# Kernel tuning notes

Hardware: AMD Instinct MI355X
Metric: run time of the kernel (lower is better)

## Reference

```python
import jax, jax.numpy as jnp
import numpy as np

B, N, M, K = 4, 8192, 2048, 8
F1, F2 = 256, 256


def _knn_idx(p1t, p2t, k):
    # p1t [B,N,3], p2t [B,M,3] -> idx [B,N,k] of k nearest points in p2t for each p1t point
    d = (jnp.sum(p1t ** 2, -1)[:, :, None]
         + jnp.sum(p2t ** 2, -1)[:, None, :]
         - 2.0 * jnp.einsum('bnc,bmc->bnm', p1t, p2t))
    _, idx = jax.lax.top_k(-d, k)
    return idx


def _gather(feat, idx):
    # feat [B,C,M], idx [B,N,K] -> [B,C,N,K]  (grouping_operation)
    return jax.vmap(lambda f, i: f[:, i])(feat, idx)


def setup_inputs() -> dict:
    key = jax.random.key(0)
    ks = jax.random.split(key, 16)
    rn = lambda k, s: jax.random.normal(k, s, dtype=jnp.float32)
    ru = lambda k, s: jax.random.uniform(k, s, dtype=jnp.float32)
    return {
        'pos1': rn(ks[0], (B, 3, N)),
        'pos2': rn(ks[1], (B, 3, M)),
        'feature1': rn(ks[2], (B, F1, N)),
        'feature2': rn(ks[3], (B, F2, M)),
        'w1_0': rn(ks[4], (128, F2 + 3)) * 0.05, 's1_0': ru(ks[5], (128,)), 'b1_0': rn(ks[6], (128,)) * 0.05,
        'w1_1': rn(ks[7], (128, 128)) * 0.05, 's1_1': ru(ks[8], (128,)), 'b1_1': rn(ks[9], (128,)) * 0.05,
        'w1_2': rn(ks[10], (256, 128)) * 0.05, 's1_2': ru(ks[11], (256,)), 'b1_2': rn(ks[12], (256,)) * 0.05,
        'w2_0': rn(ks[13], (256, 256 + F1)) * 0.05, 's2_0': ru(ks[14], (256,)), 'b2_0': rn(ks[15], (256,)) * 0.05,
    }


def reference(pos1, pos2, feature1, feature2,
              w1_0, s1_0, b1_0, w1_1, s1_1, b1_1, w1_2, s1_2, b1_2,
              w2_0, s2_0, b2_0):
    # KNN grouping (knn=True branch): neighbors of each pos1 point among pos2 points
    idx = _knn_idx(pos1.transpose(0, 2, 1), pos2.transpose(0, 2, 1), K)  # [B,N,K]
    pos2_grouped = _gather(pos2, idx)                 # [B,3,N,K]
    pos_diff = pos2_grouped - pos1[:, :, :, None]     # [B,3,N,K]
    feat2_grouped = _gather(feature2, idx)            # [B,F2,N,K]
    feat = jnp.concatenate([feat2_grouped, pos_diff], axis=1)  # [B,F2+3,N,K]
    # mlp1: 1x1 Conv2d (no bias) + BN(eval, folded scale/bias) + ReLU
    for w, s, b in ((w1_0, s1_0, b1_0), (w1_1, s1_1, b1_1), (w1_2, s1_2, b1_2)):
        feat = jax.nn.relu(jnp.einsum('oc,bcnk->bonk', w, feat)
                           * s[None, :, None, None] + b[None, :, None, None])
    feat = jnp.max(feat, axis=-1)                     # [B,256,N]
    feat = jnp.concatenate([feat, feature1], axis=1)  # [B,256+F1,N]
    # mlp2: 1x1 Conv1d (no bias) + BN + ReLU
    for w, s, b in ((w2_0, s2_0, b2_0),):
        feat = jax.nn.relu(jnp.einsum('oc,bcn->bon', w, feat)
                           * s[None, :, None] + b[None, :, None])
    return feat
```

## Files before the change

### kernel.cpp

```cpp
#include <hip/hip_runtime.h>
#include <hip/hip_bf16.h>

#define B_ 4
#define N_ 8192
#define M_ 2048
#define K_ 8

typedef __bf16 bf16x8 __attribute__((ext_vector_type(8)));
typedef __bf16 bf16x4 __attribute__((ext_vector_type(4)));
typedef float  floatx4 __attribute__((ext_vector_type(4)));
typedef unsigned long long u64k;

__global__ __launch_bounds__(256) void prep_weights(
    const float* __restrict__ w10, const float* __restrict__ w11,
    const float* __restrict__ w12, const float* __restrict__ w20,
    __bf16* __restrict__ w0p, __bf16* __restrict__ w11b,
    __bf16* __restrict__ w12b, __bf16* __restrict__ w20b)
{
  int t = blockIdx.x * 256 + threadIdx.x;
  if (t < 36864) {
    int o = t / 288, c = t - o * 288;
    w0p[t] = (c < 259) ? (__bf16)w10[o * 259 + c] : (__bf16)0.0f;
  } else if (t < 53248) {
    int i = t - 36864; w11b[i] = (__bf16)w11[i];
  } else if (t < 86016) {
    int i = t - 53248; w12b[i] = (__bf16)w12[i];
  } else if (t < 217088) {
    int i = t - 86016; w20b[i] = (__bf16)w20[i];
  }
}

__global__ __launch_bounds__(256) void transpose_cast(
    const float* __restrict__ in, __bf16* __restrict__ out, int C, int L)
{
  __shared__ float tile[32][33];
  const int b = blockIdx.z;
  const int c0 = blockIdx.y * 32, l0 = blockIdx.x * 32;
  const int tx = threadIdx.x & 31, ty = threadIdx.x >> 5;
  const float* src = in + (size_t)b * C * L;
  #pragma unroll
  for (int i = 0; i < 4; i++)
    tile[ty + 8 * i][tx] = src[(size_t)(c0 + ty + 8 * i) * L + l0 + tx];
  __syncthreads();
  __bf16* dst = out + (size_t)b * L * C;
  #pragma unroll
  for (int i = 0; i < 4; i++)
    dst[(size_t)(l0 + ty + 8 * i) * C + c0 + tx] = (__bf16)tile[tx][ty + 8 * i];
}

__device__ __forceinline__ void ce(u64k& a, u64k& b) {
  u64k lo = a < b ? a : b;
  u64k hi = a < b ? b : a;
  a = lo; b = hi;
}

__global__ __launch_bounds__(256, 4) void knn_kernel(
    const float* __restrict__ pos1, const float* __restrict__ pos2,
    u64k* __restrict__ part)
{
  __shared__ floatx4 P[1024];
  __shared__ u64k md[64][33];
  const int b = blockIdx.y;
  const int half = blockIdx.z;
  const int n0 = blockIdx.x * 64;
  const int tid = threadIdx.x;
  const int cbase = half * 1024;

  const float* p2 = pos2 + b * 3 * M_;
  for (int i = tid; i < 1024; i += 256) {
    const int c = cbase + i;
    float x = p2[c], y = p2[M_ + c], z = p2[2 * M_ + c];
    floatx4 q;
    q[0] = x; q[1] = y; q[2] = z;
    q[3] = __fadd_rn(__fadd_rn(__fmul_rn(x, x), __fmul_rn(y, y)), __fmul_rn(z, z));
    P[i] = q;
  }
  __syncthreads();

  const int p = tid >> 2, t = tid & 3;
  const int n = n0 + p;
  const float* p1 = pos1 + b * 3 * N_;
  const float x1 = p1[n], y1 = p1[N_ + n], z1 = p1[2 * N_ + n];
  const float r1 = __fadd_rn(__fadd_rn(__fmul_rn(x1, x1), __fmul_rn(y1, y1)),
                             __fmul_rn(z1, z1));

  u64k bd[8];
  #pragma unroll
  for (int r = 0; r < 8; r++) bd[r] = ~0ULL;

  for (int bb = 0; bb < 32; ++bb) {
    floatx4 q[8];
    #pragma unroll
    for (int i = 0; i < 8; i++) q[i] = P[4 * (8 * bb + i) + t];

    u64k s[8];
    #pragma unroll
    for (int i = 0; i < 8; i++) {
      float dot = __fadd_rn(__fadd_rn(__fmul_rn(x1, q[i][0]), __fmul_rn(y1, q[i][1])),
                            __fmul_rn(z1, q[i][2]));
      float d = __fsub_rn(__fadd_rn(r1, q[i][3]), __fmul_rn(2.0f, dot));
      unsigned du = __float_as_uint(d);
      unsigned k32 = du ^ ((unsigned)((int)du >> 31) | 0x80000000u);
      s[i] = ((u64k)k32 << 11) | (unsigned)(cbase + 4 * (8 * bb + i) + t);
    }

    ce(s[0], s[1]); ce(s[2], s[3]); ce(s[4], s[5]); ce(s[6], s[7]);
    ce(s[0], s[2]); ce(s[1], s[3]); ce(s[4], s[6]); ce(s[5], s[7]);
    ce(s[1], s[2]); ce(s[5], s[6]);
    ce(s[0], s[4]); ce(s[1], s[5]); ce(s[2], s[6]); ce(s[3], s[7]);
    ce(s[2], s[4]); ce(s[3], s[5]);
    ce(s[1], s[2]); ce(s[3], s[4]); ce(s[5], s[6]);

    if (s[0] < bd[7]) {
      #pragma unroll
      for (int k = 0; k < 8; k++) { u64k x = s[7 - k]; bd[k] = bd[k] < x ? bd[k] : x; }
      ce(bd[0], bd[4]); ce(bd[1], bd[5]); ce(bd[2], bd[6]); ce(bd[3], bd[7]);
      ce(bd[0], bd[2]); ce(bd[1], bd[3]); ce(bd[4], bd[6]); ce(bd[5], bd[7]);
      ce(bd[0], bd[1]); ce(bd[2], bd[3]); ce(bd[4], bd[5]); ce(bd[6], bd[7]);
    }
  }

  #pragma unroll
  for (int r = 0; r < 8; r++) md[p][t * 8 + r] = bd[r];
  __syncthreads();

  if (tid < 64) {
    int h0 = 0, h1 = 0, h2 = 0, h3 = 0;
    u64k* o = part + ((size_t)((b * 2 + half) * N_ + n0 + tid)) * 8;
    #pragma unroll
    for (int r = 0; r < 8; r++) {
      u64k k0 = md[tid][h0], k1 = md[tid][8 + h1];
      u64k k2 = md[tid][16 + h2], k3 = md[tid][24 + h3];
      u64k m01 = k0 < k1 ? k0 : k1;
      u64k m23 = k2 < k3 ? k2 : k3;
      u64k m = m01 < m23 ? m01 : m23;
      h0 += (k0 == m); h1 += (k1 == m); h2 += (k2 == m); h3 += (k3 == m);
      o[r] = m;
    }
  }
}

__global__ __launch_bounds__(256) void knn_merge(
    const u64k* __restrict__ part, int* __restrict__ idx_out)
{
  const int pt = blockIdx.x * 256 + threadIdx.x;
  const int b = pt >> 13, n = pt & (N_ - 1);
  const u64k* a0 = part + ((size_t)((b * 2 + 0) * N_ + n)) * 8;
  const u64k* a1 = part + ((size_t)((b * 2 + 1) * N_ + n)) * 8;
  u64k av[8], cv[8];
  #pragma unroll
  for (int r = 0; r < 8; r++) { av[r] = a0[r]; cv[r] = a1[r]; }
  #pragma unroll
  for (int k = 0; k < 8; k++) { u64k x = cv[7 - k]; av[k] = av[k] < x ? av[k] : x; }
  ce(av[0], av[4]); ce(av[1], av[5]); ce(av[2], av[6]); ce(av[3], av[7]);
  ce(av[0], av[2]); ce(av[1], av[3]); ce(av[4], av[6]); ce(av[5], av[7]);
  ce(av[0], av[1]); ce(av[2], av[3]); ce(av[4], av[5]); ce(av[6], av[7]);
  int* o = idx_out + (size_t)pt * 8;
  #pragma unroll
  for (int r = 0; r < 8; r++) o[r] = (int)(av[r] & 2047u);
}

template <int KSTEPS>
__device__ __forceinline__ void mfma_layer_lds(
    const __bf16* X, const __bf16* W, int wstride,
    const float* sv, const float* bv,
    __bf16* Y, int ycolbase, int c0, int lane)
{
  const int lrow = lane & 15, quad = lane >> 4;
  floatx4 acc[4][2];
  const floatx4 fz = {0.f, 0.f, 0.f, 0.f};
  #pragma unroll
  for (int pt = 0; pt < 4; pt++) { acc[pt][0] = fz; acc[pt][1] = fz; }

  bf16x8 wf0 = *(const bf16x8*)(W + (size_t)(c0 + lrow) * wstride + quad * 8);
  bf16x8 wf1 = *(const bf16x8*)(W + (size_t)(c0 + 16 + lrow) * wstride + quad * 8);
  bf16x8 xf[4];
  #pragma unroll
  for (int pt = 0; pt < 4; pt++)
    xf[pt] = *(const bf16x8*)(X + (pt * 16 + lrow) * 136 + quad * 8);

  #pragma unroll
  for (int ks = 0; ks < KSTEPS; ks++) {
    bf16x8 wn0, wn1, xn[4];
    if (ks + 1 < KSTEPS) {
      const int kn = (ks + 1) * 32 + quad * 8;
      wn0 = *(const bf16x8*)(W + (size_t)(c0 + lrow) * wstride + kn);
      wn1 = *(const bf16x8*)(W + (size_t)(c0 + 16 + lrow) * wstride + kn);
      #pragma unroll
      for (int pt = 0; pt < 4; pt++)
        xn[pt] = *(const bf16x8*)(X + (pt * 16 + lrow) * 136 + kn);
    }
    #pragma unroll
    for (int pt = 0; pt < 4; pt++) {
      acc[pt][0] = __builtin_amdgcn_mfma_f32_16x16x32_bf16(wf0, xf[pt], acc[pt][0], 0, 0, 0);
      acc[pt][1] = __builtin_amdgcn_mfma_f32_16x16x32_bf16(wf1, xf[pt], acc[pt][1], 0, 0, 0);
    }
    if (ks + 1 < KSTEPS) {
      wf0 = wn0; wf1 = wn1;
      #pragma unroll
      for (int pt = 0; pt < 4; pt++) xf[pt] = xn[pt];
    }
  }

  #pragma unroll
  for (int pt = 0; pt < 4; pt++) {
    #pragma unroll
    for (int wt = 0; wt < 2; wt++) {
      const int colg = c0 + wt * 16 + quad * 4;
      floatx4 s4 = *(const floatx4*)(sv + colg);
      floatx4 b4 = *(const floatx4*)(bv + colg);
      bf16x4 pk;
      #pragma unroll
      for (int r = 0; r < 4; r++) {
        float v = acc[pt][wt][r] * s4[r] + b4[r];
        pk[r] = (__bf16)(v > 0.f ? v : 0.f);
      }
      *(bf16x4*)(Y + (pt * 16 + lrow) * 136 + (colg - ycolbase)) = pk;
    }
  }
}

__global__ __launch_bounds__(256, 3) void mlp1_kernel(
    const float* __restrict__ pos1, const float* __restrict__ pos2,
    const int* __restrict__ idx, const __bf16* __restrict__ f2t,
    const __bf16* __restrict__ w0p, const float* __restrict__ s10, const float* __restrict__ b10,
    const __bf16* __restrict__ w11b, const float* __restrict__ s11, const float* __restrict__ b11,
    const __bf16* __restrict__ w12b, const float* __restrict__ s12, const float* __restrict__ b12,
    __bf16* __restrict__ maxed)
{
  __shared__ __align__(16) __bf16 Xs[64 * 256];
  __shared__ __align__(16) __bf16 Y0[64 * 136];
  __shared__ int mrow[64];
  __shared__ __align__(16) float dp[64][4];
  __bf16* const Y1 = Xs;

  const int b = blockIdx.y;
  const int n0 = blockIdx.x * 8;
  const int tid = threadIdx.x;
  const int wave = tid >> 6, lane = tid & 63;
  const int lrow = lane & 15, quad = lane >> 4;
  const int c0 = 32 * wave;

  if (tid < 64) {
    const int r = tid, g = r >> 3;
    const int m = idx[(b * N_ + n0) * K_ + r];
    mrow[r] = m;
    const int n = n0 + g;
    dp[r][0] = pos2[b * 3 * M_ + m]          - pos1[b * 3 * N_ + n];
    dp[r][1] = pos2[b * 3 * M_ + M_ + m]     - pos1[b * 3 * N_ + N_ + n];
    dp[r][2] = pos2[b * 3 * M_ + 2 * M_ + m] - pos1[b * 3 * N_ + 2 * N_ + n];
    dp[r][3] = 0.f;
  }
  __syncthreads();

  {
    const int r0 = wave * 16;
    const int half = lane >> 5;
    const int ch = lane & 31;
    #pragma unroll
    for (int i = 0; i < 8; i++) {
      const int r = r0 + 2 * i + half;
      const int m = mrow[r];
      const char* src = (const char*)f2t
          + (((size_t)(b * M_ + m)) << 9)
          + ((ch << 4) ^ ((r & 7) << 4));
      __builtin_amdgcn_global_load_lds(
          (const __attribute__((address_space(1))) unsigned int*)src,
          (__attribute__((address_space(3))) unsigned int*)(Xs + (r0 + 2 * i) * 256),
          16, 0, 0);
    }
  }

  bf16x8 xlast[4];
  #pragma unroll
  for (int pt = 0; pt < 4; pt++) {
    bf16x8 v = {};
    if (quad == 0) {
      floatx4 d = *(const floatx4*)(&dp[pt * 16 + lrow][0]);
      v[0] = (__bf16)d[0]; v[1] = (__bf16)d[1]; v[2] = (__bf16)d[2];
    }
    xlast[pt] = v;
  }

  bf16x8 wf0 = *(const bf16x8*)(w0p + (size_t)(c0 + lrow) * 288 + quad * 8);
  bf16x8 wf1 = *(const bf16x8*)(w0p + (size_t)(c0 + 16 + lrow) * 288 + quad * 8);

  __syncthreads();

  {
    floatx4 acc[4][2];
    const floatx4 fz = {0.f, 0.f, 0.f, 0.f};
    #pragma unroll
    for (int pt = 0; pt < 4; pt++) { acc[pt][0] = fz; acc[pt][1] = fz; }

    const int swz = (lrow & 7) << 4;
    bf16x8 xf[4];
    #pragma unroll
    for (int pt = 0; pt < 4; pt++)
      xf[pt] = *(const bf16x8*)((const char*)Xs + (pt * 16 + lrow) * 512
                                + ((quad * 16) ^ swz));

    #pragma unroll
    for (int ks = 0; ks < 9; ks++) {
      bf16x8 wn0, wn1, xn[4];
      if (ks < 8) {
        const int kn = (ks + 1) * 32 + quad * 8;
        wn0 = *(const bf16x8*)(w0p + (size_t)(c0 + lrow) * 288 + kn);
        wn1 = *(const bf16x8*)(w0p + (size_t)(c0 + 16 + lrow) * 288 + kn);
        if (ks < 7) {
          const int kb = ((ks + 1) * 64 + quad * 16) ^ swz;
          #pragma unroll
          for (int pt = 0; pt < 4; pt++)
            xn[pt] = *(const bf16x8*)((const char*)Xs + (pt * 16 + lrow) * 512 + kb);
        } else {
          #pragma unroll
          for (int pt = 0; pt < 4; pt++) xn[pt] = xlast[pt];
        }
      }
      #pragma unroll
      for (int pt = 0; pt < 4; pt++) {
        acc[pt][0] = __builtin_amdgcn_mfma_f32_16x16x32_bf16(wf0, xf[pt], acc[pt][0], 0, 0, 0);
        acc[pt][1] = __builtin_amdgcn_mfma_f32_16x16x32_bf16(wf1, xf[pt], acc[pt][1], 0, 0, 0);
      }
      if (ks < 8) {
        wf0 = wn0; wf1 = wn1;
        #pragma unroll
        for (int pt = 0; pt < 4; pt++) xf[pt] = xn[pt];
      }
    }
    #pragma unroll
    for (int pt = 0; pt < 4; pt++) {
      #pragma unroll
      for (int wt = 0; wt < 2; wt++) {
        const int colg = c0 + wt * 16 + quad * 4;
        floatx4 s4 = *(const floatx4*)(s10 + colg);
        floatx4 b4 = *(const floatx4*)(b10 + colg);
        bf16x4 pk;
        #pragma unroll
        for (int r = 0; r < 4; r++) {
          float v = acc[pt][wt][r] * s4[r] + b4[r];
          pk[r] = (__bf16)(v > 0.f ? v : 0.f);
        }
        *(bf16x4*)(Y0 + (pt * 16 + lrow) * 136 + colg) = pk;
      }
    }
  }
  __syncthreads();

  mfma_layer_lds<4>(Y0, w11b, 128, s11, b11, Y1, 0, c0, lane);
  __syncthreads();

  #pragma unroll
  for (int p = 0; p < 2; p++) {
    mfma_layer_lds<4>(Y1, w12b, 128, s12, b12, Y0, 128 * p, 128 * p + c0, lane);
    __syncthreads();
    if (tid < 128) {
      const int g = tid >> 4, cb = (tid & 15) * 8;
      bf16x8 v0 = *(const bf16x8*)(Y0 + (g * 8) * 136 + cb);
      float fmx[8];
      #pragma unroll
      for (int j = 0; j < 8; j++) fmx[j] = (float)v0[j];
      #pragma unroll
      for (int k = 1; k < 8; k++) {
        bf16x8 v = *(const bf16x8*)(Y0 + (g * 8 + k) * 136 + cb);
        #pragma unroll
        for (int j = 0; j < 8; j++) {
          float f = (float)v[j];
          fmx[j] = f > fmx[j] ? f : fmx[j];
        }
      }
      bf16x8 o;
      #pragma unroll
      for (int j = 0; j < 8; j++) o[j] = (__bf16)fmx[j];
      *(bf16x8*)(maxed + ((size_t)(b * N_ + n0 + g)) * 256 + 128 * p + cb) = o;
    }
    __syncthreads();
  }
}

__global__ __launch_bounds__(256, 6) void mlp2_kernel(
    const __bf16* __restrict__ maxed, const __bf16* __restrict__ f1t,
    const __bf16* __restrict__ w20b, const float* __restrict__ s20,
    const float* __restrict__ b20, float* __restrict__ out)
{
  const int rows0 = blockIdx.x * 32;
  const int b = rows0 >> 13;
  const int nbase = rows0 & (N_ - 1);
  const int tid = threadIdx.x;
  const int wave = tid >> 6, lane = tid & 63;
  const int lrow = lane & 15, quad = lane >> 4;
  const int c0 = 128 * blockIdx.y + 32 * wave;
  const floatx4 fz = {0.f, 0.f, 0.f, 0.f};

  floatx4 acc[2][2];
  acc[0][0] = fz; acc[0][1] = fz; acc[1][0] = fz; acc[1][1] = fz;

  auto aptr = [&](int ks, int mt) -> const __bf16* {
    const int k = ks * 32 + quad * 8;
    return (ks < 8) ? (maxed + (size_t)(rows0 + mt * 16 + lrow) * 256 + k)
                    : (f1t + (size_t)(rows0 + mt * 16 + lrow) * 256 + (k - 256));
  };

  bf16x8 w0 = *(const bf16x8*)(w20b + (size_t)(c0 + lrow) * 512 + quad * 8);
  bf16x8 w1 = *(const bf16x8*)(w20b + (size_t)(c0 + 16 + lrow) * 512 + quad * 8);
  bf16x8 a0 = *(const bf16x8*)aptr(0, 0);
  bf16x8 a1 = *(const bf16x8*)aptr(0, 1);

  #pragma unroll
  for (int ks = 0; ks < 16; ks++) {
    bf16x8 wn0, wn1, an0, an1;
    if (ks < 15) {
      const int kn = (ks + 1) * 32 + quad * 8;
      wn0 = *(const bf16x8*)(w20b + (size_t)(c0 + lrow) * 512 + kn);
      wn1 = *(const bf16x8*)(w20b + (size_t)(c0 + 16 + lrow) * 512 + kn);
      an0 = *(const bf16x8*)aptr(ks + 1, 0);
      an1 = *(const bf16x8*)aptr(ks + 1, 1);
    }
    acc[0][0] = __builtin_amdgcn_mfma_f32_16x16x32_bf16(a0, w0, acc[0][0], 0, 0, 0);
    acc[0][1] = __builtin_amdgcn_mfma_f32_16x16x32_bf16(a0, w1, acc[0][1], 0, 0, 0);
    acc[1][0] = __builtin_amdgcn_mfma_f32_16x16x32_bf16(a1, w0, acc[1][0], 0, 0, 0);
    acc[1][1] = __builtin_amdgcn_mfma_f32_16x16x32_bf16(a1, w1, acc[1][1], 0, 0, 0);
    if (ks < 15) { w0 = wn0; w1 = wn1; a0 = an0; a1 = an1; }
  }

  #pragma unroll
  for (int ct = 0; ct < 2; ct++) {
    const int col = c0 + ct * 16 + lrow;
    const float s = s20[col];
    const float bb = b20[col];
    #pragma unroll
    for (int mt = 0; mt < 2; mt++) {
      floatx4 pk;
      #pragma unroll
      for (int r = 0; r < 4; r++) {
        float v = acc[mt][ct][r] * s + bb;
        pk[r] = v > 0.f ? v : 0.f;
      }
      const int n = nbase + mt * 16 + quad * 4;
      *(floatx4*)(out + ((size_t)(b * 256 + col)) * N_ + n) = pk;
    }
  }
}

extern "C" void kernel_launch(void* const* d_in, const int* in_sizes, int n_in,
                              void* d_out, int out_size, void* d_ws, size_t ws_size,
                              hipStream_t stream)
{
  const float* pos1     = (const float*)d_in[0];
  const float* pos2     = (const float*)d_in[1];
  const float* feature1 = (const float*)d_in[2];
  const float* feature2 = (const float*)d_in[3];
  const float* w1_0 = (const float*)d_in[4];
  const float* s1_0 = (const float*)d_in[5];
  const float* b1_0 = (const float*)d_in[6];
  const float* w1_1 = (const float*)d_in[7];
  const float* s1_1 = (const float*)d_in[8];
  const float* b1_1 = (const float*)d_in[9];
  const float* w1_2 = (const float*)d_in[10];
  const float* s1_2 = (const float*)d_in[11];
  const float* b1_2 = (const float*)d_in[12];
  const float* w2_0 = (const float*)d_in[13];
  const float* s2_0 = (const float*)d_in[14];
  const float* b2_0 = (const float*)d_in[15];

  char* ws = (char*)d_ws;
  int*    idx   = (int*)(ws);
  __bf16* f2t   = (__bf16*)(ws + 1048576);
  __bf16* f1t   = (__bf16*)(ws + 5242880);
  __bf16* maxed = (__bf16*)(ws + 22020096);
  __bf16* w0p   = (__bf16*)(ws + 38797312);
  __bf16* w11b  = (__bf16*)(ws + 38871040);
  __bf16* w12b  = (__bf16*)(ws + 38903808);
  __bf16* w20b  = (__bf16*)(ws + 38969344);
  u64k*   part  = (u64k*)(ws + 22020096);

  prep_weights<<<dim3(848), 256, 0, stream>>>(w1_0, w1_1, w1_2, w2_0,
                                              w0p, w11b, w12b, w20b);
  transpose_cast<<<dim3(M_ / 32, 8, B_), 256, 0, stream>>>(feature2, f2t, 256, M_);
  transpose_cast<<<dim3(N_ / 32, 8, B_), 256, 0, stream>>>(feature1, f1t, 256, N_);
  knn_kernel<<<dim3(N_ / 64, B_, 2), 256, 0, stream>>>(pos1, pos2, part);
  knn_merge<<<dim3(N_ * B_ / 256), 256, 0, stream>>>(part, idx);
  mlp1_kernel<<<dim3(N_ / 8, B_), 256, 0, stream>>>(
      pos1, pos2, idx, f2t, w0p, s1_0, b1_0, w11b, s1_1, b1_1, w12b, s1_2, b1_2, maxed);
  mlp2_kernel<<<dim3(1024, 2), 256, 0, stream>>>(maxed, f1t, w20b, s2_0, b2_0,
                                                 (float*)d_out);
}
```

Baseline: 340.0 us.

## Shrink mlp1 LDS footprint with XOR-swizzled buffers and raise occupancy

Replaces the padded 136-stride intermediate LDS buffers with XOR-swizzled 256-byte rows carved out of the existing Xs buffer. This removes the separate Y0, mrow and dp shared arrays, so launch bounds can go from 3 to 5 blocks per CU. The neighbor indices and position differences are now loaded straight from global memory into registers, which drops one barrier. The per-point max-pool is done by each wave on its own columns without block-wide barriers. The trade-off is an extra barrier before layer-0 writes, because Y0 now aliases Xs, and possible register pressure at the higher occupancy target.

Result: slower. 346.9 us (+2.1%).

```diff
diff --git a/kernel.cpp b/kernel.cpp
--- a/kernel.cpp
+++ b/kernel.cpp
@@ -161,7 +161,7 @@
 }
 
 template <int KSTEPS>
-__device__ __forceinline__ void mfma_layer_lds(
+__device__ __forceinline__ void mfma_layer_swz(
     const __bf16* X, const __bf16* W, int wstride,
     const float* sv, const float* bv,
     __bf16* Y, int ycolbase, int c0, int lane)
@@ -176,8 +176,11 @@
   bf16x8 wf1 = *(const bf16x8*)(W + (size_t)(c0 + 16 + lrow) * wstride + quad * 8);
   bf16x8 xf[4];
   #pragma unroll
-  for (int pt = 0; pt < 4; pt++)
-    xf[pt] = *(const bf16x8*)(X + (pt * 16 + lrow) * 136 + quad * 8);
+  for (int pt = 0; pt < 4; pt++) {
+    const int row = pt * 16 + lrow;
+    xf[pt] = *(const bf16x8*)((const char*)X + row * 256
+                              + ((quad * 16) ^ ((row & 7) << 4)));
+  }
 
   #pragma unroll
   for (int ks = 0; ks < KSTEPS; ks++) {
@@ -187,8 +190,11 @@
       wn0 = *(const bf16x8*)(W + (size_t)(c0 + lrow) * wstride + kn);
       wn1 = *(const bf16x8*)(W + (size_t)(c0 + 16 + lrow) * wstride + kn);
       #pragma unroll
-      for (int pt = 0; pt < 4; pt++)
-        xn[pt] = *(const bf16x8*)(X + (pt * 16 + lrow) * 136 + kn);
+      for (int pt = 0; pt < 4; pt++) {
+        const int row = pt * 16 + lrow;
+        xn[pt] = *(const bf16x8*)((const char*)X + row * 256
+                                  + (((ks + 1) * 64 + quad * 16) ^ ((row & 7) << 4)));
+      }
     }
     #pragma unroll
     for (int pt = 0; pt < 4; pt++) {
@@ -215,12 +221,15 @@
         float v = acc[pt][wt][r] * s4[r] + b4[r];
         pk[r] = (__bf16)(v > 0.f ? v : 0.f);
       }
-      *(bf16x4*)(Y + (pt * 16 + lrow) * 136 + (colg - ycolbase)) = pk;
-    }
-  }
-}
-
-__global__ __launch_bounds__(256, 3) void mlp1_kernel(
+      const int row = pt * 16 + lrow;
+      const int cb = (colg - ycolbase) * 2;
+      *(bf16x4*)((char*)Y + row * 256
+                 + ((cb & ~15) ^ ((row & 7) << 4)) + (cb & 15)) = pk;
+    }
+  }
+}
+
+__global__ __launch_bounds__(256, 5) void mlp1_kernel(
     const float* __restrict__ pos1, const float* __restrict__ pos2,
     const int* __restrict__ idx, const __bf16* __restrict__ f2t,
     const __bf16* __restrict__ w0p, const float* __restrict__ s10, const float* __restrict__ b10,
@@ -229,10 +238,8 @@
     __bf16* __restrict__ maxed)
 {
   __shared__ __align__(16) __bf16 Xs[64 * 256];
-  __shared__ __align__(16) __bf16 Y0[64 * 136];
-  __shared__ int mrow[64];
-  __shared__ __align__(16) float dp[64][4];
   __bf16* const Y1 = Xs;
+  __bf16* const Y0 = Xs + 32 * 256;
 
   const int b = blockIdx.y;
   const int n0 = blockIdx.x * 8;
@@ -240,29 +247,21 @@
   const int wave = tid >> 6, lane = tid & 63;
   const int lrow = lane & 15, quad = lane >> 4;
   const int c0 = 32 * wave;
-
-  if (tid < 64) {
-    const int r = tid, g = r >> 3;
-    const int m = idx[(b * N_ + n0) * K_ + r];
-    mrow[r] = m;
-    const int n = n0 + g;
-    dp[r][0] = pos2[b * 3 * M_ + m]          - pos1[b * 3 * N_ + n];
-    dp[r][1] = pos2[b * 3 * M_ + M_ + m]     - pos1[b * 3 * N_ + N_ + n];
-    dp[r][2] = pos2[b * 3 * M_ + 2 * M_ + m] - pos1[b * 3 * N_ + 2 * N_ + n];
-    dp[r][3] = 0.f;
-  }
-  __syncthreads();
+  const int idxbase = (b * N_ + n0) * K_;
 
   {
     const int r0 = wave * 16;
-    const int half = lane >> 5;
+    const int hf = lane >> 5;
     const int ch = lane & 31;
+    int mr[8];
+    #pragma unroll
+    for (int i = 0; i < 8; i++)
+      mr[i] = idx[idxbase + r0 + 2 * i + hf];
     #pragma unroll
     for (int i = 0; i < 8; i++) {
-      const int r = r0 + 2 * i + half;
-      const int m = mrow[r];
+      const int r = r0 + 2 * i + hf;
       const char* src = (const char*)f2t
-          + (((size_t)(b * M_ + m)) << 9)
+          + (((size_t)(b * M_ + mr[i])) << 9)
           + ((ch << 4) ^ ((r & 7) << 4));
       __builtin_amdgcn_global_load_lds(
           (const __attribute__((address_space(1))) unsigned int*)src,
@@ -273,13 +272,19 @@
 
   bf16x8 xlast[4];
   #pragma unroll
-  for (int pt = 0; pt < 4; pt++) {
-    bf16x8 v = {};
-    if (quad == 0) {
-      floatx4 d = *(const floatx4*)(&dp[pt * 16 + lrow][0]);
-      v[0] = (__bf16)d[0]; v[1] = (__bf16)d[1]; v[2] = (__bf16)d[2];
-    }
-    xlast[pt] = v;
+  for (int pt = 0; pt < 4; pt++) { bf16x8 v = {}; xlast[pt] = v; }
+  if (quad == 0) {
+    #pragma unroll
+    for (int pt = 0; pt < 4; pt++) {
+      const int r = pt * 16 + lrow;
+      const int m = idx[idxbase + r];
+      const int n = n0 + (r >> 3);
+      bf16x8 v = {};
+      v[0] = (__bf16)(pos2[b * 3 * M_ + m]          - pos1[b * 3 * N_ + n]);
+      v[1] = (__bf16)(pos2[b * 3 * M_ + M_ + m]     - pos1[b * 3 * N_ + N_ + n]);
+      v[2] = (__bf16)(pos2[b * 3 * M_ + 2 * M_ + m] - pos1[b * 3 * N_ + 2 * N_ + n]);
+      xlast[pt] = v;
+    }
   }
 
   bf16x8 wf0 = *(const bf16x8*)(w0p + (size_t)(c0 + lrow) * 288 + quad * 8);
@@ -287,8 +292,8 @@
 
   __syncthreads();
 
+  floatx4 acc[4][2];
   {
-    floatx4 acc[4][2];
     const floatx4 fz = {0.f, 0.f, 0.f, 0.f};
     #pragma unroll
     for (int pt = 0; pt < 4; pt++) { acc[pt][0] = fz; acc[pt][1] = fz; }
@@ -328,41 +333,50 @@
         for (int pt = 0; pt < 4; pt++) xf[pt] = xn[pt];
       }
     }
-    #pragma unroll
-    for (int pt = 0; pt < 4; pt++) {
-      #pragma unroll
-      for (int wt = 0; wt < 2; wt++) {
-        const int colg = c0 + wt * 16 + quad * 4;
-        floatx4 s4 = *(const floatx4*)(s10 + colg);
-        floatx4 b4 = *(const floatx4*)(b10 + colg);
-        bf16x4 pk;
+  }
+
+  __syncthreads();
+
+  #pragma unroll
+  for (int pt = 0; pt < 4; pt++) {
+    #pragma unroll
+    for (int wt = 0; wt < 2; wt++) {
+      const int colg = c0 + wt * 16 + quad * 4;
+      floatx4 s4 = *(const floatx4*)(s10 + colg);
+      floatx4 b4 = *(const floatx4*)(b10 + colg);
+      bf16x4 pk;
+      #pragma unroll
+      for (int r = 0; r < 4; r++) {
+        float v = acc[pt][wt][r] * s4[r] + b4[r];
+        pk[r] = (__bf16)(v > 0.f ? v : 0.f);
+      }
+      const int row = pt * 16 + lrow;
+      const int cb = colg * 2;
+      *(bf16x4*)((char*)Y0 + row * 256
+                 + ((cb & ~15) ^ ((row & 7) << 4)) + (cb & 15)) = pk;
+    }
+  }
+  __syncthreads();
+
+  mfma_layer_swz<4>(Y0, w11b, 128, s11, b11, Y1, 0, c0, lane);
+  __syncthreads();
+
+  #pragma unroll
+  for (int p = 0; p < 2; p++) {
+    mfma_layer_swz<4>(Y1, w12b, 128, s12, b12, Y0, 128 * p, 128 * p + c0, lane);
+    if (lane < 32) {
+      const int pnt = lane >> 2, c8 = lane & 3;
+      const int cbb = 2 * c0 + 16 * c8;
+      float fmx[8];
+      {
+        bf16x8 v = *(const bf16x8*)((const char*)Y0 + (pnt * 8) * 256 + (cbb ^ 0));
         #pragma unroll
-        for (int r = 0; r < 4; r++) {
-          float v = acc[pt][wt][r] * s4[r] + b4[r];
-          pk[r] = (__bf16)(v > 0.f ? v : 0.f);
-        }
-        *(bf16x4*)(Y0 + (pt * 16 + lrow) * 136 + colg) = pk;
-      }
-    }
-  }
-  __syncthreads();
-
-  mfma_layer_lds<4>(Y0, w11b, 128, s11, b11, Y1, 0, c0, lane);
-  __syncthreads();
-
-  #pragma unroll
-  for (int p = 0; p < 2; p++) {
-    mfma_layer_lds<4>(Y1, w12b, 128, s12, b12, Y0, 128 * p, 128 * p + c0, lane);
-    __syncthreads();
-    if (tid < 128) {
-      const int g = tid >> 4, cb = (tid & 15) * 8;
-      bf16x8 v0 = *(const bf16x8*)(Y0 + (g * 8) * 136 + cb);
-      float fmx[8];
-      #pragma unroll
-      for (int j = 0; j < 8; j++) fmx[j] = (float)v0[j];
+        for (int j = 0; j < 8; j++) fmx[j] = (float)v[j];
+      }
       #pragma unroll
       for (int k = 1; k < 8; k++) {
-        bf16x8 v = *(const bf16x8*)(Y0 + (g * 8 + k) * 136 + cb);
+        bf16x8 v = *(const bf16x8*)((const char*)Y0 + (pnt * 8 + k) * 256
+                                    + (cbb ^ (k << 4)));
         #pragma unroll
         for (int j = 0; j < 8; j++) {
           float f = (float)v[j];
@@ -372,9 +386,8 @@
       bf16x8 o;
       #pragma unroll
       for (int j = 0; j < 8; j++) o[j] = (__bf16)fmx[j];
-      *(bf16x8*)(maxed + ((size_t)(b * N_ + n0 + g)) * 256 + 128 * p + cb) = o;
-    }
-    __syncthreads();
+      *(bf16x8*)(maxed + ((size_t)(b * N_ + n0 + pnt)) * 256 + 128 * p + c0 + c8 * 8) = o;
+    }
   }
 }
 
```
